# Performance work log

Measured on AMD Instinct MI355X. Metric: run time of the kernel, lower is better.

The kernel has to match this reference:

```python
import jax, jax.numpy as jnp
import numpy as np

TOP_X = 3
M = 10
K = 10
BETA = 2.0
EPS = 1e-12  # matches torch F.normalize eps


def setup_inputs() -> dict:
    key = jax.random.key(0)
    kq, kd = jax.random.split(key)
    query_features = jax.random.normal(kq, (128, 512), dtype=jnp.float32)
    db = jax.random.normal(kd, (100000, 512), dtype=jnp.float32)
    return {"query_features": query_features, "db": db}


def _get_top_k(q, db, k):
    # Dense inner-product kNN: q [n, D], db [N, D] -> ([n, k, D], [n, k], [n, k])
    s = q @ db.T                      # [n, N]
    ts, ti = jax.lax.top_k(s, k)      # [n, k]
    return db[ti], ts, ti


def reference(query_features, db):
    B, D = query_features.shape
    # First-level retrieval: top-M neighbors of each query
    top_m, _, top_m_ids = _get_top_k(query_features, db, M)       # [B, M, D]
    # Query expansion: elementwise max over query + its top K-1 neighbors
    top_k = top_m[:, : K - 1]                                     # [B, K-1, D]
    query_top_k = jnp.max(
        jnp.concatenate((query_features[:, None, :], top_k), axis=1), axis=1
    )                                                              # [B, D]
    # Second-level retrieval: top-K neighbors of each of the B*M candidates
    top_k_m, top_k_m_scores, _ = _get_top_k(top_m.reshape(-1, D), db, K)
    top_k_m = top_k_m.reshape(B, M, K, D)
    top_k_m_scores = top_k_m_scores.reshape(B, M, K)
    # Prepend the query itself (weight 1) to each neighbor set
    exp_q = jnp.broadcast_to(query_features[:, None, None, :], (B, M, 1, D))
    top_k_m = jnp.concatenate((exp_q, top_k_m), axis=2)            # [B, M, K+1, D]
    ones = jnp.ones((B, M, 1), dtype=query_features.dtype)
    scores_all = jnp.concatenate((ones, top_k_m_scores), axis=2)   # [B, M, K+1]
    # Weighted neighbor aggregation (SuperGlobal refinement)
    weights = scores_all * BETA
    weighted_sum = jnp.einsum('bmkd,bmk->bmd', top_k_m, weights)   # [B, M, D]
    norm_factor = 1.0 + jnp.sum(weights, axis=2, keepdims=True)    # [B, M, 1]
    top_m_refined = weighted_sum / norm_factor
    # L2 normalize refined candidates and expanded query
    top_m_refined = top_m_refined / jnp.clip(
        jnp.linalg.norm(top_m_refined, axis=-1, keepdims=True), EPS)
    query_top_k = query_top_k / jnp.clip(
        jnp.linalg.norm(query_top_k, axis=-1, keepdims=True), EPS)
    # Rerank scores
    score_1 = jnp.einsum('bmd,bd->bm', top_m_refined, query_features)
    score_2 = jnp.einsum('bmd,bd->bm', top_m_refined, query_top_k)
    final_scores = (score_1 + score_2) * 0.5                        # [B, M]
    top_x_scores, top_x_indices = jax.lax.top_k(final_scores, TOP_X)
    top_x_ids = jnp.take_along_axis(top_m_ids, top_x_indices, axis=1)
    return (top_x_ids, top_x_scores)
```

## Files before the change

kernel.cpp:

```cpp
#include <hip/hip_runtime.h>
#include <math.h>

#define NQ    128
#define ND    512
#define NDB   100000
#define NDBP  100096
#define MM    10
#define KK    10
#define TOPX  3
#define R2    (NQ * MM)

#define QB1    128
#define NB1    64
#define NCH1   (NDBP / NB1)
#define QB2    256
#define NB2    128
#define NCH2   (NDBP / NB2)
#define NQT2   (R2 / QB2)
#define KT     64
#define NKIT   (ND / KT)

#define Z0    3.125f
#define QSC   32.0f
#define CAP   384
#define NROWT (NQ + R2)

typedef int i32x4 __attribute__((ext_vector_type(4)));

#define PIPE_BAR(VM) asm volatile("s_waitcnt vmcnt(" #VM ")\n\ts_barrier" ::: "memory")
#define LGKM_BAR()   asm volatile("s_waitcnt lgkmcnt(0)\n\ts_barrier" ::: "memory")

__device__ __forceinline__ void gload_lds16(const void* gsrc, void* ldst) {
    __builtin_amdgcn_global_load_lds(
        (const __attribute__((address_space(1))) unsigned int*)gsrc,
        (__attribute__((address_space(3))) unsigned int*)ldst, 16, 0, 0);
}

__device__ __forceinline__ signed char f2i8(float x) {
    int v = (int)rintf(x * QSC);
    v = v > 127 ? 127 : v;
    v = v < -127 ? -127 : v;
    return (signed char)v;
}

__global__ __launch_bounds__(256) void prep_q_kernel(
    const float* __restrict__ src, signed char* __restrict__ dst,
    int* __restrict__ thrI, int* __restrict__ cnt)
{
    const int row = blockIdx.x;
    const int t = (int)threadIdx.x;
    __shared__ float red[4];
    const float a = src[(size_t)row * ND + t];
    const float b = src[(size_t)row * ND + t + 256];
    dst[(size_t)row * ND + t] = f2i8(a);
    dst[(size_t)row * ND + t + 256] = f2i8(b);
    float ss = a * a + b * b;
    for (int off = 32; off; off >>= 1) ss += __shfl_xor(ss, off);
    if ((t & 63) == 0) red[t >> 6] = ss;
    __syncthreads();
    if (t == 0) {
        const float tot = red[0] + red[1] + red[2] + red[3];
        thrI[row] = (int)(QSC * QSC * Z0 * sqrtf(tot));
        cnt[row] = 0;
    }
}

__global__ __launch_bounds__(256) void gemm1f_kernel(
    const signed char* __restrict__ Qb,
    const float* __restrict__ Df,
    signed char* __restrict__ DbOut,
    const int* __restrict__ thrI,
    int* __restrict__ candCnt, int* __restrict__ candId)
{
    __shared__ char dlds[32768];
    __shared__ char qlds[2][8192];
    __shared__ int thrS[QB1];

    const int tid = (int)threadIdx.x;
    const int ln = tid & 63;
    const int wv = tid >> 6;
    const int wr = wv >> 1;
    const int wc = wv & 1;
    const int n0 = blockIdx.x * NB1;

    if (tid < QB1) thrS[tid] = thrI[tid];

    auto stageQ = [&](int kc, int buf) {
#pragma unroll
        for (int c = 0; c < 2; ++c) {
            const int U = c * 256 + tid;
            const int r = U >> 2;
            const int u = (U & 3) ^ ((r >> 1) & 3);
            gload_lds16(Qb + (size_t)r * ND + kc + u * 16,
                        qlds[buf] + U * 16);
        }
    };
    stageQ(0, 0);
    stageQ(KT, 1);

#pragma unroll 2
    for (int pass = 0; pass < 8; ++pass) {
        const int o = pass * 4096 + tid * 16;
        const int r = o >> 9;
        const int kk = o & 511;
        const int u16 = kk >> 4;
        const int ks = u16 >> 2;
        const int us = u16 & 3;
        const int gn = n0 + r;
        union { signed char cc[16]; i32x4 v; } w;
        if (gn < NDB) {
            const float4* p = (const float4*)(Df + (size_t)gn * ND + kk);
#pragma unroll
            for (int j = 0; j < 4; ++j) {
                const float4 f = p[j];
                w.cc[j * 4 + 0] = f2i8(f.x);
                w.cc[j * 4 + 1] = f2i8(f.y);
                w.cc[j * 4 + 2] = f2i8(f.z);
                w.cc[j * 4 + 3] = f2i8(f.w);
            }
        } else {
#pragma unroll
            for (int j = 0; j < 16; ++j) w.cc[j] = 0;
        }
        *(i32x4*)(dlds + ks * 4096 + r * 64 + ((us ^ ((r >> 1) & 3)) * 16)) = w.v;
        *(i32x4*)(DbOut + (size_t)gn * ND + kk) = w.v;
    }
    __syncthreads();

    i32x4 acc[4][2] = {};
#pragma unroll
    for (int it = 0; it < NKIT; ++it) {
        if (it < NKIT - 1) PIPE_BAR(2); else PIPE_BAR(0);
        const int buf = it & 1;
        const char* Qt = qlds[buf];
        const char* Dt = dlds + it * 4096;
        i32x4 a[4], b[2];
#pragma unroll
        for (int qt = 0; qt < 4; ++qt) {
            const int r = wr * 64 + qt * 16 + (ln & 15);
            const int u = (ln >> 4) ^ ((r >> 1) & 3);
            a[qt] = *(const i32x4*)(Qt + r * 64 + u * 16);
        }
#pragma unroll
        for (int nt = 0; nt < 2; ++nt) {
            const int r = wc * 32 + nt * 16 + (ln & 15);
            const int u = (ln >> 4) ^ ((r >> 1) & 3);
            b[nt] = *(const i32x4*)(Dt + r * 64 + u * 16);
        }
        __builtin_amdgcn_s_setprio(1);
#pragma unroll
        for (int qt = 0; qt < 4; ++qt)
#pragma unroll
            for (int nt = 0; nt < 2; ++nt)
                acc[qt][nt] = __builtin_amdgcn_mfma_i32_16x16x64_i8(
                    a[qt], b[nt], acc[qt][nt], 0, 0, 0);
        __builtin_amdgcn_s_setprio(0);
        LGKM_BAR();
        if (it + 2 < NKIT) stageQ((it + 2) * KT, buf);
    }

    const int lg = ln >> 4;
    const int lc = ln & 15;
#pragma unroll
    for (int qt = 0; qt < 4; ++qt) {
#pragma unroll
        for (int c = 0; c < 4; ++c) {
            const int rloc = wr * 64 + qt * 16 + lg * 4 + c;
            const int T = thrS[rloc];
#pragma unroll
            for (int nt = 0; nt < 2; ++nt) {
                const int v = acc[qt][nt][c];
                if (v > T) {
                    const int n = n0 + wc * 32 + nt * 16 + lc;
                    if (n < NDB) {
                        const int slot = atomicAdd(&candCnt[rloc], 1);
                        if (slot < CAP) candId[(size_t)rloc * CAP + slot] = n;
                    }
                }
            }
        }
    }
}

__global__ __launch_bounds__(512) void gemm2s_kernel(
    const signed char* __restrict__ Qb,
    const signed char* __restrict__ Db,
    const int* __restrict__ thrI,
    int* __restrict__ candCnt, int* __restrict__ candId)
{
    const int bid = (int)blockIdx.x;
    const int xcd = bid & 7;
    const int slot = bid >> 3;
    const int nch_x = (xcd < 6) ? 98 : 97;
    if (slot >= nch_x * 5) return;
    const int cstart = (xcd < 6) ? 98 * xcd : 98 * 6 + 97 * (xcd - 6);
    const int chunk = cstart + slot / 5;
    const int qtile = slot % 5;

    __shared__ char lds[49152];
    __shared__ int thrS[QB2];

    const int tid = (int)threadIdx.x;
    const int ln = tid & 63;
    const int wv = tid >> 6;
    const int wr = wv >> 1;
    const int wc = wv & 1;
    const int q0 = qtile * QB2;
    const int n0 = chunk * NB2;

    if (tid < QB2) thrS[tid] = thrI[q0 + tid];

    i32x4 acc[4][4] = {};

    auto stageQ = [&](int kc, int buf) {
#pragma unroll
        for (int c = 0; c < 2; ++c) {
            const int U = c * 512 + tid;
            const int r = U >> 2;
            const int u = (U & 3) ^ ((r >> 1) & 3);
            gload_lds16(Qb + (size_t)(q0 + r) * ND + kc + u * 16,
                        lds + buf * 24576 + U * 16);
        }
    };
    auto stageD = [&](int kc, int buf) {
        const int U = tid;
        const int r = U >> 2;
        const int u = (U & 3) ^ ((r >> 1) & 3);
        gload_lds16(Db + (size_t)(n0 + r) * ND + kc + u * 16,
                    lds + buf * 24576 + 16384 + U * 16);
    };
    auto compute = [&](int buf) {
        const char* Qt = lds + buf * 24576;
        const char* Dt = Qt + 16384;
        i32x4 a[4], b[4];
#pragma unroll
        for (int qt = 0; qt < 4; ++qt) {
            const int r = wr * 64 + qt * 16 + (ln & 15);
            const int u = (ln >> 4) ^ ((r >> 1) & 3);
            a[qt] = *(const i32x4*)(Qt + r * 64 + u * 16);
        }
#pragma unroll
        for (int nt = 0; nt < 4; ++nt) {
            const int r = wc * 64 + nt * 16 + (ln & 15);
            const int u = (ln >> 4) ^ ((r >> 1) & 3);
            b[nt] = *(const i32x4*)(Dt + r * 64 + u * 16);
        }
        __builtin_amdgcn_s_setprio(1);
#pragma unroll
        for (int qt = 0; qt < 4; ++qt)
#pragma unroll
            for (int nt = 0; nt < 4; ++nt)
                acc[qt][nt] = __builtin_amdgcn_mfma_i32_16x16x64_i8(
                    a[qt], b[nt], acc[qt][nt], 0, 0, 0);
        __builtin_amdgcn_s_setprio(0);
    };

    __syncthreads();
    stageQ(0, 0); stageD(0, 0);
    stageQ(KT, 1); stageD(KT, 1);
#pragma unroll
    for (int it = 0; it < NKIT; ++it) {
        if (it < NKIT - 1) PIPE_BAR(3); else PIPE_BAR(0);
        const int buf = it & 1;
        compute(buf);
        LGKM_BAR();
        if (it + 2 < NKIT) { stageQ((it + 2) * KT, buf); stageD((it + 2) * KT, buf); }
    }

    const int lg = ln >> 4;
    const int lc = ln & 15;
#pragma unroll
    for (int qt = 0; qt < 4; ++qt) {
#pragma unroll
        for (int c = 0; c < 4; ++c) {
            const int rloc = wr * 64 + qt * 16 + lg * 4 + c;
            const int row = q0 + rloc;
            const int T = thrS[rloc];
#pragma unroll
            for (int nt = 0; nt < 4; ++nt) {
                const int v = acc[qt][nt][c];
                if (v > T) {
                    const int n = n0 + wc * 64 + nt * 16 + lc;
                    if (n < NDB) {
                        const int slot2 = atomicAdd(&candCnt[row], 1);
                        if (slot2 < CAP) candId[(size_t)row * CAP + slot2] = n;
                    }
                }
            }
        }
    }
}

__global__ __launch_bounds__(512) void gemm2_cvt_kernel(
    const signed char* __restrict__ Qb, const float* __restrict__ Df,
    const int* __restrict__ thrI, int* __restrict__ candCnt, int* __restrict__ candId,
    int qrows)
{
    __shared__ char lds[49152];
    __shared__ int thrS[QB2];
    const int tid = (int)threadIdx.x;
    const int ln = tid & 63;
    const int wv = tid >> 6;
    const int wr = wv >> 1;
    const int wc = wv & 1;
    const int q0 = blockIdx.x * QB2;
    const int n0 = blockIdx.y * NB2;
    if (tid < QB2 && q0 + tid < qrows) thrS[tid] = thrI[q0 + tid];
    else if (tid < QB2) thrS[tid] = 0x7fffffff;

    i32x4 acc[4][4] = {};
    auto stageQ = [&](int kc, int buf) {
#pragma unroll
        for (int c = 0; c < 2; ++c) {
            const int U = c * 512 + tid;
            const int r = U >> 2;
            const int u = (U & 3) ^ ((r >> 1) & 3);
            const int gq = q0 + r;
            if (gq < qrows)
                gload_lds16(Qb + (size_t)gq * ND + kc + u * 16,
                            lds + buf * 24576 + U * 16);
            else
                *(i32x4*)(lds + buf * 24576 + U * 16) = i32x4{0, 0, 0, 0};
        }
    };
    auto stageDcvt = [&](int kc, int buf) {
        const int U = tid;
        const int r = U >> 2;
        const int u = (U & 3) ^ ((r >> 1) & 3);
        const int gn = n0 + r;
        union { signed char cc[16]; i32x4 v; } w;
        if (gn < NDB) {
#pragma unroll
            for (int j = 0; j < 4; ++j) {
                const float4 f = *(const float4*)(Df + (size_t)gn * ND + kc + u * 16 + j * 4);
                w.cc[j * 4 + 0] = f2i8(f.x);
                w.cc[j * 4 + 1] = f2i8(f.y);
                w.cc[j * 4 + 2] = f2i8(f.z);
                w.cc[j * 4 + 3] = f2i8(f.w);
            }
        } else {
#pragma unroll
            for (int j = 0; j < 16; ++j) w.cc[j] = 0;
        }
        *(i32x4*)(lds + buf * 24576 + 16384 + U * 16) = w.v;
    };
    stageQ(0, 0); stageDcvt(0, 0);
    for (int it = 0; it < NKIT; ++it) {
        const int buf = it & 1;
        __syncthreads();
        if (it + 1 < NKIT) { stageQ((it + 1) * KT, buf ^ 1); stageDcvt((it + 1) * KT, buf ^ 1); }
        const char* Qt = lds + buf * 24576;
        const char* Dt = Qt + 16384;
        i32x4 a[4], b[4];
#pragma unroll
        for (int qt = 0; qt < 4; ++qt) {
            const int r = wr * 64 + qt * 16 + (ln & 15);
            const int u = (ln >> 4) ^ ((r >> 1) & 3);
            a[qt] = *(const i32x4*)(Qt + r * 64 + u * 16);
        }
#pragma unroll
        for (int nt = 0; nt < 4; ++nt) {
            const int r = wc * 64 + nt * 16 + (ln & 15);
            const int u = (ln >> 4) ^ ((r >> 1) & 3);
            b[nt] = *(const i32x4*)(Dt + r * 64 + u * 16);
        }
#pragma unroll
        for (int qt = 0; qt < 4; ++qt)
#pragma unroll
            for (int nt = 0; nt < 4; ++nt)
                acc[qt][nt] = __builtin_amdgcn_mfma_i32_16x16x64_i8(
                    a[qt], b[nt], acc[qt][nt], 0, 0, 0);
        __syncthreads();
    }
    const int lg = ln >> 4;
    const int lc = ln & 15;
#pragma unroll
    for (int qt = 0; qt < 4; ++qt) {
#pragma unroll
        for (int c = 0; c < 4; ++c) {
            const int rloc = wr * 64 + qt * 16 + lg * 4 + c;
            const int row = q0 + rloc;
            if (row >= qrows) continue;
            const int T = thrS[rloc];
#pragma unroll
            for (int nt = 0; nt < 4; ++nt) {
                const int v = acc[qt][nt][c];
                if (v > T) {
                    const int n = n0 + wc * 64 + nt * 16 + lc;
                    if (n < NDB) {
                        const int slot = atomicAdd(&candCnt[row], 1);
                        if (slot < CAP) candId[(size_t)row * CAP + slot] = n;
                    }
                }
            }
        }
    }
}

__global__ __launch_bounds__(256) void rescore_fuse_kernel(
    const float* __restrict__ Qf,
    const float* __restrict__ db,
    const int* __restrict__ candCnt, const int* __restrict__ candId,
    int* __restrict__ s1I,
    float* __restrict__ q2f, signed char* __restrict__ q2i8,
    float* __restrict__ qtk,
    int* __restrict__ thrI2, int* __restrict__ cnt2)
{
    const int b = blockIdx.x;
    const int tid = (int)threadIdx.x;
    const int ln = tid & 63;
    const int wv = tid >> 6;

    __shared__ float qs[ND];
    __shared__ float sc[CAP];
    __shared__ int   sid[CAP];
    __shared__ float rbs[4];
    __shared__ int   rbi[4], rbsl[4];
    __shared__ int   topI[MM];
    __shared__ float red[11][4];

    qs[tid] = Qf[(size_t)b * ND + tid];
    qs[tid + 256] = Qf[(size_t)b * ND + tid + 256];
    const int nc = min(candCnt[b], CAP);
    for (int i = tid; i < CAP; i += 256) { sc[i] = -INFINITY; sid[i] = 0x7fffffff; }
    __syncthreads();

    for (int i = wv; i < nc; i += 4) {
        const int id = candId[(size_t)b * CAP + i];
        const float4* d4 = (const float4*)(db + (size_t)id * ND);
        const float4 qa = *(const float4*)&qs[ln * 8];
        const float4 qb = *(const float4*)&qs[ln * 8 + 4];
        const float4 da = d4[ln * 2];
        const float4 dbv = d4[ln * 2 + 1];
        float s = qa.x * da.x + qa.y * da.y + qa.z * da.z + qa.w * da.w
                + qb.x * dbv.x + qb.y * dbv.y + qb.z * dbv.z + qb.w * dbv.w;
        for (int off = 32; off; off >>= 1) s += __shfl_xor(s, off);
        if (ln == 0) { sc[i] = s; sid[i] = id; }
    }
    __syncthreads();

    for (int it = 0; it < KK; ++it) {
        float bs = -INFINITY;
        int bid = 0x7fffffff, bsl = -1;
        for (int i = tid; i < nc; i += 256) {
            const float s = sc[i];
            if (s > bs || (s == bs && sid[i] < bid)) { bs = s; bid = sid[i]; bsl = i; }
        }
        for (int off = 32; off; off >>= 1) {
            const float os = __shfl_xor(bs, off);
            const int oi = __shfl_xor(bid, off);
            const int osl = __shfl_xor(bsl, off);
            if (os > bs || (os == bs && oi < bid)) { bs = os; bid = oi; bsl = osl; }
        }
        if (ln == 0) { rbs[wv] = bs; rbi[wv] = bid; rbsl[wv] = bsl; }
        __syncthreads();
        if (tid == 0) {
            float fb = -INFINITY; int fi = 0x7fffffff, fs = -1;
#pragma unroll
            for (int w = 0; w < 4; ++w) {
                if (rbs[w] > fb || (rbs[w] == fb && rbi[w] < fi)) {
                    fb = rbs[w]; fi = rbi[w]; fs = rbsl[w];
                }
            }
            const int idw = (fi == 0x7fffffff) ? 0 : fi;
            s1I[b * MM + it] = idw;
            topI[it] = idw;
            if (fs >= 0) sc[fs] = -INFINITY;
        }
        __syncthreads();
    }

    const float q0v = qs[tid];
    const float q1v = qs[tid + 256];
    float mx0 = q0v, mx1 = q1v;
    float ssq[MM];
#pragma unroll
    for (int m = 0; m < MM; ++m) {
        const int id = topI[m];
        const float v0 = db[(size_t)id * ND + tid];
        const float v1 = db[(size_t)id * ND + tid + 256];
        const size_t rowo = (size_t)(b * MM + m) * ND;
        q2f[rowo + tid] = v0;
        q2f[rowo + tid + 256] = v1;
        q2i8[rowo + tid] = f2i8(v0);
        q2i8[rowo + tid + 256] = f2i8(v1);
        ssq[m] = v0 * v0 + v1 * v1;
        if (m < KK - 1) { mx0 = fmaxf(mx0, v0); mx1 = fmaxf(mx1, v1); }
    }
    float sqq = mx0 * mx0 + mx1 * mx1;
#pragma unroll
    for (int m = 0; m < MM; ++m) {
        float s = ssq[m];
        for (int off = 32; off; off >>= 1) s += __shfl_xor(s, off);
        if (ln == 0) red[m][wv] = s;
    }
    for (int off = 32; off; off >>= 1) sqq += __shfl_xor(sqq, off);
    if (ln == 0) red[10][wv] = sqq;
    __syncthreads();
    if (tid < MM) {
        const float tot = red[tid][0] + red[tid][1] + red[tid][2] + red[tid][3];
        thrI2[b * MM + tid] = (int)(QSC * QSC * Z0 * sqrtf(tot));
        cnt2[b * MM + tid] = 0;
    }
    const float tq = red[10][0] + red[10][1] + red[10][2] + red[10][3];
    const float inv = 1.0f / fmaxf(sqrtf(tq), 1e-12f);
    qtk[(size_t)b * ND + tid] = mx0 * inv;
    qtk[(size_t)b * ND + tid + 256] = mx1 * inv;
}

__global__ __launch_bounds__(256) void rescore_refine_kernel(
    const float* __restrict__ Qf,
    const float* __restrict__ q,
    const float* __restrict__ qtk,
    const float* __restrict__ db,
    const int* __restrict__ candCnt, const int* __restrict__ candId,
    float* __restrict__ finalS)
{
    const int row = blockIdx.x;
    const int b = row / MM;
    const int tid = (int)threadIdx.x;
    const int ln = tid & 63;
    const int wv = tid >> 6;

    __shared__ float qs[ND];
    __shared__ float sc[CAP];
    __shared__ int   sid[CAP];
    __shared__ float rbs[4];
    __shared__ int   rbi[4], rbsl[4];
    __shared__ float topS[KK];
    __shared__ int   topI[KK];
    __shared__ float red[3][4];

    qs[tid] = Qf[(size_t)row * ND + tid];
    qs[tid + 256] = Qf[(size_t)row * ND + tid + 256];
    const int nc = min(candCnt[row], CAP);
    for (int i = tid; i < CAP; i += 256) { sc[i] = -INFINITY; sid[i] = 0x7fffffff; }
    __syncthreads();

    for (int i = wv; i < nc; i += 4) {
        const int id = candId[(size_t)row * CAP + i];
        const float4* d4 = (const float4*)(db + (size_t)id * ND);
        const float4 qa = *(const float4*)&qs[ln * 8];
        const float4 qb = *(const float4*)&qs[ln * 8 + 4];
        const float4 da = d4[ln * 2];
        const float4 dbv = d4[ln * 2 + 1];
        float s = qa.x * da.x + qa.y * da.y + qa.z * da.z + qa.w * da.w
                + qb.x * dbv.x + qb.y * dbv.y + qb.z * dbv.z + qb.w * dbv.w;
        for (int off = 32; off; off >>= 1) s += __shfl_xor(s, off);
        if (ln == 0) { sc[i] = s; sid[i] = id; }
    }
    __syncthreads();

    for (int it = 0; it < KK; ++it) {
        float bs = -INFINITY;
        int bid = 0x7fffffff, bsl = -1;
        for (int i = tid; i < nc; i += 256) {
            const float s = sc[i];
            if (s > bs || (s == bs && sid[i] < bid)) { bs = s; bid = sid[i]; bsl = i; }
        }
        for (int off = 32; off; off >>= 1) {
            const float os = __shfl_xor(bs, off);
            const int oi = __shfl_xor(bid, off);
            const int osl = __shfl_xor(bsl, off);
            if (os > bs || (os == bs && oi < bid)) { bs = os; bid = oi; bsl = osl; }
        }
        if (ln == 0) { rbs[wv] = bs; rbi[wv] = bid; rbsl[wv] = bsl; }
        __syncthreads();
        if (tid == 0) {
            float fb = -INFINITY; int fi = 0x7fffffff, fs = -1;
#pragma unroll
            for (int w = 0; w < 4; ++w) {
                if (rbs[w] > fb || (rbs[w] == fb && rbi[w] < fi)) {
                    fb = rbs[w]; fi = rbi[w]; fs = rbsl[w];
                }
            }
            if (!(fb > -INFINITY)) { fb = 0.f; fi = 0; }
            topS[it] = fb;
            topI[it] = (fi == 0x7fffffff) ? 0 : fi;
            if (fs >= 0) sc[fs] = -INFINITY;
        }
        __syncthreads();
    }

    float ssum = 0.f;
#pragma unroll
    for (int m = 0; m < KK; ++m) ssum += topS[m];
    const float nf = 3.f + 2.f * ssum;

    const float q0v = q[(size_t)b * ND + tid];
    const float q1v = q[(size_t)b * ND + tid + 256];
    float w0 = 2.f * q0v;
    float w1 = 2.f * q1v;
#pragma unroll
    for (int m = 0; m < KK; ++m) {
        const int id = topI[m];
        const float w = 2.f * topS[m];
        w0 = fmaf(w, db[(size_t)id * ND + tid], w0);
        w1 = fmaf(w, db[(size_t)id * ND + tid + 256], w1);
    }
    w0 /= nf;
    w1 /= nf;

    float s_n = w0 * w0 + w1 * w1;
    float s_1 = w0 * q0v + w1 * q1v;
    float s_2 = w0 * qtk[(size_t)b * ND + tid] + w1 * qtk[(size_t)b * ND + tid + 256];
    for (int off = 32; off; off >>= 1) {
        s_n += __shfl_xor(s_n, off);
        s_1 += __shfl_xor(s_1, off);
        s_2 += __shfl_xor(s_2, off);
    }
    if (ln == 0) { red[0][wv] = s_n; red[1][wv] = s_1; red[2][wv] = s_2; }
    __syncthreads();
    if (tid == 0) {
        const float tn = red[0][0] + red[0][1] + red[0][2] + red[0][3];
        const float t1 = red[1][0] + red[1][1] + red[1][2] + red[1][3];
        const float t2 = red[2][0] + red[2][1] + red[2][2] + red[2][3];
        const float inv = 1.0f / fmaxf(sqrtf(tn), 1e-12f);
        finalS[row] = 0.5f * (t1 * inv + t2 * inv);
    }
}

__global__ __launch_bounds__(64) void final_topk_kernel(
    const float* __restrict__ finalS, const int* __restrict__ s1I,
    float* __restrict__ out)
{
    const int b = blockIdx.x * 64 + (int)threadIdx.x;
    if (b >= NQ) return;
    float s[MM];
#pragma unroll
    for (int m = 0; m < MM; ++m) s[m] = finalS[b * MM + m];
#pragma unroll
    for (int x = 0; x < TOPX; ++x) {
        float bs = -INFINITY;
        int bm = 0;
#pragma unroll
        for (int m = 0; m < MM; ++m) {
            if (s[m] > bs) { bs = s[m]; bm = m; }
        }
        out[b * TOPX + x] = (float)s1I[b * MM + bm];
        out[NQ * TOPX + b * TOPX + x] = bs;
        s[bm] = -INFINITY;
    }
}

extern "C" void kernel_launch(void* const* d_in, const int* in_sizes, int n_in,
                              void* d_out, int out_size, void* d_ws, size_t ws_size,
                              hipStream_t stream)
{
    const float* q = (const float*)d_in[0];
    const float* db = (const float*)d_in[1];
    float* out = (float*)d_out;

    char* ws = (char*)d_ws;
    size_t off = 0;
    auto alloc = [&](size_t bytes) -> void* {
        void* p = ws + off;
        off += (bytes + 255) & ~(size_t)255;
        return p;
    };
    signed char* qi8  = (signed char*)alloc((size_t)NQ * ND);
    signed char* q2i8 = (signed char*)alloc((size_t)R2 * ND);
    float* q2f  = (float*)alloc(sizeof(float) * (size_t)R2 * ND);
    float* qtk  = (float*)alloc(sizeof(float) * NQ * ND);
    int*   thrI = (int*)alloc(sizeof(int) * NROWT);
    int*   cnt  = (int*)alloc(sizeof(int) * NROWT);
    int*   cid  = (int*)alloc(sizeof(int) * (size_t)NROWT * CAP);
    int*   s1I  = (int*)alloc(sizeof(int) * NQ * MM);
    float* fS   = (float*)alloc(sizeof(float) * NQ * MM);
    signed char* dbi8 = (signed char*)alloc((size_t)NDBP * ND);
    const bool pathA = (ws_size >= off);

    prep_q_kernel<<<NQ, 256, 0, stream>>>(q, qi8, thrI, cnt);

    if (pathA) {
        gemm1f_kernel<<<NCH1, 256, 0, stream>>>(qi8, db, dbi8, thrI, cnt, cid);
    } else {
        gemm2_cvt_kernel<<<dim3(1, NCH2), 512, 0, stream>>>(
            qi8, db, thrI, cnt, cid, NQ);
    }

    rescore_fuse_kernel<<<NQ, 256, 0, stream>>>(
        q, db, cnt, cid, s1I, q2f, q2i8, qtk, thrI + NQ, cnt + NQ);

    if (pathA)
        gemm2s_kernel<<<3920, 512, 0, stream>>>(
            q2i8, dbi8, thrI + NQ, cnt + NQ, cid + (size_t)NQ * CAP);
    else
        gemm2_cvt_kernel<<<dim3(NQT2, NCH2), 512, 0, stream>>>(
            q2i8, db, thrI + NQ, cnt + NQ, cid + (size_t)NQ * CAP, R2);

    rescore_refine_kernel<<<R2, 256, 0, stream>>>(
        q2f, q, qtk, db, cnt + NQ, cid + (size_t)NQ * CAP, fS);

    final_topk_kernel<<<(NQ + 63) / 64, 64, 0, stream>>>(fS, s1I, out);
    (void)in_sizes; (void)n_in; (void)out_size;
}
```

Measured before the change: 249.7 us.

## Split DB int8 conversion into standalone kernel and widen first-level GEMM tile

```diff
diff --git a/kernel.cpp b/kernel.cpp
--- a/kernel.cpp
+++ b/kernel.cpp
@@ -11,14 +11,11 @@
 #define R2    (NQ * MM)
 
 #define QB1    128
-#define NB1    64
-#define NCH1   (NDBP / NB1)
 #define QB2    256
-#define NB2    128
-#define NCH2   (NDBP / NB2)
-#define NQT2   (R2 / QB2)
+#define NB     128
 #define KT     64
 #define NKIT   (ND / KT)
+#define NCHUNK (NDBP / NB)
 
 #define Z0    3.125f
 #define QSC   32.0f
@@ -41,6 +38,28 @@
     v = v > 127 ? 127 : v;
     v = v < -127 ? -127 : v;
     return (signed char)v;
+}
+
+__global__ __launch_bounds__(256) void cvt_db_kernel(
+    const float* __restrict__ db, signed char* __restrict__ out)
+{
+    const size_t i = ((size_t)blockIdx.x * 256 + threadIdx.x) * 16;
+    if (i >= (size_t)NDBP * ND) return;
+    union { signed char c[16]; i32x4 v; } u;
+    if (i + 16 <= (size_t)NDB * ND) {
+#pragma unroll
+        for (int j = 0; j < 4; ++j) {
+            const float4 f = *(const float4*)(db + i + j * 4);
+            u.c[j * 4 + 0] = f2i8(f.x);
+            u.c[j * 4 + 1] = f2i8(f.y);
+            u.c[j * 4 + 2] = f2i8(f.z);
+            u.c[j * 4 + 3] = f2i8(f.w);
+        }
+    } else {
+#pragma unroll
+        for (int j = 0; j < 16; ++j) u.c[j] = 0;
+    }
+    *(i32x4*)(out + i) = u.v;
 }
 
 __global__ __launch_bounds__(256) void prep_q_kernel(
@@ -65,15 +84,13 @@
     }
 }
 
-__global__ __launch_bounds__(256) void gemm1f_kernel(
+__global__ __launch_bounds__(256) void gemm1_kernel(
     const signed char* __restrict__ Qb,
-    const float* __restrict__ Df,
-    signed char* __restrict__ DbOut,
+    const signed char* __restrict__ Db,
     const int* __restrict__ thrI,
     int* __restrict__ candCnt, int* __restrict__ candId)
 {
-    __shared__ char dlds[32768];
-    __shared__ char qlds[2][8192];
+    __shared__ char lds[32768];
     __shared__ int thrS[QB1];
 
     const int tid = (int)threadIdx.x;
@@ -81,9 +98,11 @@
     const int wv = tid >> 6;
     const int wr = wv >> 1;
     const int wc = wv & 1;
-    const int n0 = blockIdx.x * NB1;
+    const int n0 = blockIdx.x * NB;
 
     if (tid < QB1) thrS[tid] = thrI[tid];
+
+    i32x4 acc[4][4] = {};
 
     auto stageQ = [&](int kc, int buf) {
 #pragma unroll
@@ -92,49 +111,23 @@
             const int r = U >> 2;
             const int u = (U & 3) ^ ((r >> 1) & 3);
             gload_lds16(Qb + (size_t)r * ND + kc + u * 16,
-                        qlds[buf] + U * 16);
-        }
-    };
-    stageQ(0, 0);
-    stageQ(KT, 1);
-
-#pragma unroll 2
-    for (int pass = 0; pass < 8; ++pass) {
-        const int o = pass * 4096 + tid * 16;
-        const int r = o >> 9;
-        const int kk = o & 511;
-        const int u16 = kk >> 4;
-        const int ks = u16 >> 2;
-        const int us = u16 & 3;
-        const int gn = n0 + r;
-        union { signed char cc[16]; i32x4 v; } w;
-        if (gn < NDB) {
-            const float4* p = (const float4*)(Df + (size_t)gn * ND + kk);
-#pragma unroll
-            for (int j = 0; j < 4; ++j) {
-                const float4 f = p[j];
-                w.cc[j * 4 + 0] = f2i8(f.x);
-                w.cc[j * 4 + 1] = f2i8(f.y);
-                w.cc[j * 4 + 2] = f2i8(f.z);
-                w.cc[j * 4 + 3] = f2i8(f.w);
-            }
-        } else {
-#pragma unroll
-            for (int j = 0; j < 16; ++j) w.cc[j] = 0;
-        }
-        *(i32x4*)(dlds + ks * 4096 + r * 64 + ((us ^ ((r >> 1) & 3)) * 16)) = w.v;
-        *(i32x4*)(DbOut + (size_t)gn * ND + kk) = w.v;
-    }
-    __syncthreads();
-
-    i32x4 acc[4][2] = {};
-#pragma unroll
-    for (int it = 0; it < NKIT; ++it) {
-        if (it < NKIT - 1) PIPE_BAR(2); else PIPE_BAR(0);
-        const int buf = it & 1;
-        const char* Qt = qlds[buf];
-        const char* Dt = dlds + it * 4096;
-        i32x4 a[4], b[2];
+                        lds + buf * 16384 + U * 16);
+        }
+    };
+    auto stageD = [&](int kc, int buf) {
+#pragma unroll
+        for (int c = 0; c < 2; ++c) {
+            const int U = c * 256 + tid;
+            const int r = U >> 2;
+            const int u = (U & 3) ^ ((r >> 1) & 3);
+            gload_lds16(Db + (size_t)(n0 + r) * ND + kc + u * 16,
+                        lds + buf * 16384 + 8192 + U * 16);
+        }
+    };
+    auto compute = [&](int buf) {
+        const char* Qt = lds + buf * 16384;
+        const char* Dt = Qt + 8192;
+        i32x4 a[4], b[4];
 #pragma unroll
         for (int qt = 0; qt < 4; ++qt) {
             const int r = wr * 64 + qt * 16 + (ln & 15);
@@ -142,8 +135,8 @@
             a[qt] = *(const i32x4*)(Qt + r * 64 + u * 16);
         }
 #pragma unroll
-        for (int nt = 0; nt < 2; ++nt) {
-            const int r = wc * 32 + nt * 16 + (ln & 15);
+        for (int nt = 0; nt < 4; ++nt) {
+            const int r = wc * 64 + nt * 16 + (ln & 15);
             const int u = (ln >> 4) ^ ((r >> 1) & 3);
             b[nt] = *(const i32x4*)(Dt + r * 64 + u * 16);
         }
@@ -151,12 +144,22 @@
 #pragma unroll
         for (int qt = 0; qt < 4; ++qt)
 #pragma unroll
-            for (int nt = 0; nt < 2; ++nt)
+            for (int nt = 0; nt < 4; ++nt)
                 acc[qt][nt] = __builtin_amdgcn_mfma_i32_16x16x64_i8(
                     a[qt], b[nt], acc[qt][nt], 0, 0, 0);
         __builtin_amdgcn_s_setprio(0);
+    };
+
+    __syncthreads();
+    stageQ(0, 0); stageD(0, 0);
+    stageQ(KT, 1); stageD(KT, 1);
+#pragma unroll
+    for (int it = 0; it < NKIT; ++it) {
+        if (it < NKIT - 1) PIPE_BAR(4); else PIPE_BAR(0);
+        const int buf = it & 1;
+        compute(buf);
         LGKM_BAR();
-        if (it + 2 < NKIT) stageQ((it + 2) * KT, buf);
+        if (it + 2 < NKIT) { stageQ((it + 2) * KT, buf); stageD((it + 2) * KT, buf); }
     }
 
     const int lg = ln >> 4;
@@ -168,10 +171,10 @@
             const int rloc = wr * 64 + qt * 16 + lg * 4 + c;
             const int T = thrS[rloc];
 #pragma unroll
-            for (int nt = 0; nt < 2; ++nt) {
+            for (int nt = 0; nt < 4; ++nt) {
                 const int v = acc[qt][nt][c];
                 if (v > T) {
-                    const int n = n0 + wc * 32 + nt * 16 + lc;
+                    const int n = n0 + wc * 64 + nt * 16 + lc;
                     if (n < NDB) {
                         const int slot = atomicAdd(&candCnt[rloc], 1);
                         if (slot < CAP) candId[(size_t)rloc * CAP + slot] = n;
@@ -206,7 +209,7 @@
     const int wr = wv >> 1;
     const int wc = wv & 1;
     const int q0 = qtile * QB2;
-    const int n0 = chunk * NB2;
+    const int n0 = chunk * NB;
 
     if (tid < QB2) thrS[tid] = thrI[q0 + tid];
 
@@ -304,7 +307,7 @@
     const int wr = wv >> 1;
     const int wc = wv & 1;
     const int q0 = blockIdx.x * QB2;
-    const int n0 = blockIdx.y * NB2;
+    const int n0 = blockIdx.y * NB;
     if (tid < QB2 && q0 + tid < qrows) thrS[tid] = thrI[q0 + tid];
     else if (tid < QB2) thrS[tid] = 0x7fffffff;
 
@@ -673,9 +676,10 @@
     prep_q_kernel<<<NQ, 256, 0, stream>>>(q, qi8, thrI, cnt);
 
     if (pathA) {
-        gemm1f_kernel<<<NCH1, 256, 0, stream>>>(qi8, db, dbi8, thrI, cnt, cid);
+        cvt_db_kernel<<<(int)(((size_t)NDBP * ND / 16 + 255) / 256), 256, 0, stream>>>(db, dbi8);
+        gemm1_kernel<<<NCHUNK, 256, 0, stream>>>(qi8, dbi8, thrI, cnt, cid);
     } else {
-        gemm2_cvt_kernel<<<dim3(1, NCH2), 512, 0, stream>>>(
+        gemm2_cvt_kernel<<<dim3(1, NCHUNK), 512, 0, stream>>>(
             qi8, db, thrI, cnt, cid, NQ);
     }
 
@@ -686,7 +690,7 @@
         gemm2s_kernel<<<3920, 512, 0, stream>>>(
             q2i8, dbi8, thrI + NQ, cnt + NQ, cid + (size_t)NQ * CAP);
     else
-        gemm2_cvt_kernel<<<dim3(NQT2, NCH2), 512, 0, stream>>>(
+        gemm2_cvt_kernel<<<dim3(R2 / QB2, NCHUNK), 512, 0, stream>>>(
             q2i8, db, thrI + NQ, cnt + NQ, cid + (size_t)NQ * CAP, R2);
 
     rescore_refine_kernel<<<R2, 256, 0, stream>>>(
```

Result: slower. 261.1 us (+4.6%).
